# Optimization experiments

Measured on AMD Instinct MI355X. Metric: run time of the kernel, lower is better.

Reference implementation:

```python
import jax, jax.numpy as jnp
import numpy as np

B, T, D, E, TOP_K = 4, 4096, 1024, 8, 2
CAPACITY_FACTOR = 1.5


def setup_inputs() -> dict:
    key = jax.random.key(0)
    k1, k2, k3 = jax.random.split(key, 3)
    x = jax.random.normal(k1, (B, T, D), dtype=jnp.float32)
    Wr = jax.random.normal(k2, (E, D), dtype=jnp.float32) * 0.02   # router weight [E, D]
    We = jax.random.normal(k3, (E, D, D), dtype=jnp.float32) * 0.02  # per-expert dense [E, D, D]
    return {"x": x, "Wr": Wr, "We": We}


def reference(x, Wr, We):
    Bb, Tt, Dd = x.shape
    Ee = Wr.shape[0]
    K = TOP_K
    C = int(Tt * K / Ee * CAPACITY_FACTOR) + 1  # max_tokens_per_expert

    # Router + fused top-k softmax (triton_topk_softmax semantics)
    logits = jnp.einsum('btd,ed->bte', x, Wr)                 # [B, T, E]
    top_vals, top_idx = jax.lax.top_k(logits, K)              # [B, T, K]
    w = jax.nn.softmax(top_vals, axis=-1)                     # [B, T, K]

    # Position of each (token, k) slot inside its expert's capacity buffer,
    # assigned in (t, k) order -- matches the sequential counter in _build_position_map.
    flat_e = top_idx.reshape(Bb, Tt * K)                      # [B, T*K]
    oh = jax.nn.one_hot(flat_e, Ee, dtype=jnp.int32)          # [B, T*K, E]
    pos_all = jnp.cumsum(oh, axis=1) - oh                     # count of earlier slots per expert
    pos = jnp.take_along_axis(pos_all, flat_e[..., None], axis=-1)[..., 0]  # [B, T*K]
    keep = pos < C                                            # capacity drop

    # Scatter tokens into [B, E, C, D] capacity buffers (triton_expert_scatter)
    b_idx = jnp.arange(Bb, dtype=jnp.int32)[:, None]
    dst = (b_idx * Ee + flat_e) * C + pos                     # flat buffer index
    dst = jnp.where(keep, dst, Bb * Ee * C).reshape(-1)       # out-of-range -> dropped
    x_rep = jnp.repeat(x, K, axis=1).reshape(-1, Dd)          # [B*T*K, D]
    buf = jnp.zeros((Bb * Ee * C, Dd), dtype=x.dtype).at[dst].add(x_rep, mode='drop')
    expert_in = buf.reshape(Bb, Ee, C, Dd)

    # expert_fn: per-expert dense layer (grouped GEMM)
    expert_out = jnp.einsum('becd,edf->becf', expert_in, We)  # [B, E, C, D]

    # Gather back + weighted combine (triton_expert_gather)
    gathered = jnp.take(expert_out.reshape(Bb * Ee * C, Dd), dst, axis=0,
                        mode='fill', fill_value=0.0)          # dropped slots -> 0
    gathered = gathered.reshape(Bb, Tt, K, Dd)
    out = jnp.einsum('btk,btkd->btd', w, gathered)            # [B, T, D]
    return out
```

## Files before the change

kernel.cpp:

```cpp
#include <hip/hip_runtime.h>
#include <hip/hip_bf16.h>
#include <math.h>

#define B_ 4
#define T_ 4096
#define D_ 1024
#define E_ 8
#define K_ 2
#define C_ 1537

typedef short bf16x8 __attribute__((ext_vector_type(8)));
typedef float f32x4 __attribute__((ext_vector_type(4)));

__device__ __forceinline__ unsigned short f2bf(float f) {
    union { float f; unsigned int u; } c; c.f = f;
    unsigned int u = c.u;
    return (unsigned short)((u + 0x7fffu + ((u >> 16) & 1u)) >> 16);
}
__device__ __forceinline__ float bf2f(unsigned short u) {
    union { unsigned int i; float f; } c; c.i = ((unsigned int)u) << 16;
    return c.f;
}
__device__ __forceinline__ void ldsdma16(const void* g, void* l) {
    __builtin_amdgcn_global_load_lds((const __attribute__((address_space(1))) void*)g,
                                     (__attribute__((address_space(3))) void*)l, 16, 0, 0);
}

__global__ __launch_bounds__(256) void router_kernel(
    const float* __restrict__ x, const float* __restrict__ Wr,
    unsigned short* __restrict__ xbf, int* __restrict__ top_e,
    float* __restrict__ wbuf) {
    __shared__ float wr_s[E_ * D_];
    int tid = threadIdx.x;
    const float4* wr4 = (const float4*)Wr;
    float4* wrs4 = (float4*)wr_s;
    #pragma unroll
    for (int i = 0; i < 8; i++) wrs4[tid + i * 256] = wr4[tid + i * 256];
    __syncthreads();

    int wave = tid >> 6, lane = tid & 63;
    int h5 = (lane >> 5) & 1, h4 = (lane >> 4) & 1, h3 = (lane >> 3) & 1;

    for (int tt = 0; tt < 4; tt++) {
        int token = blockIdx.x * 16 + wave * 4 + tt;
        const float4* xr = (const float4*)(x + (size_t)token * D_) + lane * 4;
        float xs[16];
        #pragma unroll
        for (int i = 0; i < 4; i++) {
            float4 v = xr[i];
            xs[i * 4 + 0] = v.x; xs[i * 4 + 1] = v.y;
            xs[i * 4 + 2] = v.z; xs[i * 4 + 3] = v.w;
        }
        unsigned short xb[16];
        #pragma unroll
        for (int i = 0; i < 16; i++) xb[i] = f2bf(xs[i]);
        uint4* dst = (uint4*)(xbf + (size_t)token * D_ + lane * 16);
        dst[0] = ((uint4*)xb)[0];
        dst[1] = ((uint4*)xb)[1];

        double acc[E_];
        #pragma unroll
        for (int e = 0; e < E_; e++) {
            const float* wp = wr_s + e * D_ + lane * 16;
            double a = 0.0;
            #pragma unroll
            for (int i = 0; i < 16; i++) a += (double)xs[i] * (double)wp[i];
            acc[e] = a;
        }
        double r4[4];
        #pragma unroll
        for (int i = 0; i < 4; i++) {
            double send = h5 ? acc[i] : acc[4 + i];
            double keep = h5 ? acc[4 + i] : acc[i];
            r4[i] = keep + __shfl_xor(send, 32, 64);
        }
        double r2[2];
        #pragma unroll
        for (int i = 0; i < 2; i++) {
            double send = h4 ? r4[i] : r4[2 + i];
            double keep = h4 ? r4[2 + i] : r4[i];
            r2[i] = keep + __shfl_xor(send, 16, 64);
        }
        double r1;
        {
            double send = h3 ? r2[0] : r2[1];
            double keep = h3 ? r2[1] : r2[0];
            r1 = keep + __shfl_xor(send, 8, 64);
        }
        r1 += __shfl_xor(r1, 4, 64);
        r1 += __shfl_xor(r1, 2, 64);
        r1 += __shfl_xor(r1, 1, 64);
        double le[E_];
        #pragma unroll
        for (int e = 0; e < E_; e++) le[e] = __shfl(r1, e << 3, 64);

        if (lane == 0) {
            int e0 = 0; double v0 = le[0];
            #pragma unroll
            for (int e = 1; e < E_; e++) if (le[e] > v0) { v0 = le[e]; e0 = e; }
            int e1 = -1; double v1 = -1.0e300;
            #pragma unroll
            for (int e = 0; e < E_; e++) if (e != e0 && le[e] > v1) { v1 = le[e]; e1 = e; }
            double ex = exp(v1 - v0);
            top_e[token * 2 + 0] = e0;
            top_e[token * 2 + 1] = e1;
            wbuf[token * 2 + 0] = (float)(1.0 / (1.0 + ex));
            wbuf[token * 2 + 1] = (float)(ex / (1.0 + ex));
        }
    }
}

__global__ __launch_bounds__(256) void wt_kernel(const float* __restrict__ We,
                                                 unsigned short* __restrict__ wtbf) {
    __shared__ unsigned short tile[64][65];
    int e = blockIdx.x >> 8;
    int t = blockIdx.x & 255;
    int d0 = (t >> 4) * 64, f0 = (t & 15) * 64;
    const float* src = We + ((size_t)e * D_ + d0) * D_ + f0;
    int tid = threadIdx.x;
    #pragma unroll
    for (int i = 0; i < 16; i++) {
        int idx = tid + i * 256;
        int r = idx >> 6, c = idx & 63;
        tile[r][c] = f2bf(src[(size_t)r * D_ + c]);
    }
    __syncthreads();
    unsigned short* dstp = wtbf + ((size_t)e * D_ + f0) * D_ + d0;
    #pragma unroll
    for (int i = 0; i < 16; i++) {
        int idx = tid + i * 256;
        int r = idx >> 6, c = idx & 63;
        dstp[(size_t)r * D_ + c] = tile[c][r];
    }
}

__global__ __launch_bounds__(256) void scan_kernel(const int* __restrict__ top_e,
                                                   int* __restrict__ list,
                                                   int* __restrict__ count,
                                                   unsigned char* __restrict__ keep8) {
    int b = blockIdx.x, tid = threadIdx.x;
    const int per = 32;
    __shared__ int cnt[256][9];
    int local[E_];
    #pragma unroll
    for (int e = 0; e < E_; e++) local[e] = 0;
    const int* te = top_e + (size_t)b * 8192 + tid * per;
    int evals[32];
    for (int i = 0; i < per; i++) { evals[i] = te[i]; local[evals[i]]++; }
    #pragma unroll
    for (int e = 0; e < E_; e++) cnt[tid][e] = local[e];
    __syncthreads();

    int wave = tid >> 6, lane = tid & 63;
    #pragma unroll
    for (int ee = 0; ee < 2; ee++) {
        int e = wave * 2 + ee;
        int s0 = cnt[lane * 4 + 0][e], s1 = cnt[lane * 4 + 1][e];
        int s2 = cnt[lane * 4 + 2][e], s3 = cnt[lane * 4 + 3][e];
        int tot = s0 + s1 + s2 + s3;
        int s = tot;
        #pragma unroll
        for (int off = 1; off < 64; off <<= 1) {
            int t2 = __shfl_up(s, off, 64);
            if (lane >= off) s += t2;
        }
        int base = s - tot;
        cnt[lane * 4 + 0][e] = base;
        cnt[lane * 4 + 1][e] = base + s0;
        cnt[lane * 4 + 2][e] = base + s0 + s1;
        cnt[lane * 4 + 3][e] = base + s0 + s1 + s2;
        if (lane == 63) count[b * E_ + e] = min(s, C_);
    }
    __syncthreads();

    int base[E_];
    #pragma unroll
    for (int e = 0; e < E_; e++) base[e] = cnt[tid][e];
    int* lst = list + (size_t)b * E_ * C_;
    unsigned char* kp = keep8 + (size_t)b * 8192;
    for (int i = 0; i < per; i++) {
        int ev = evals[i];
        int p = base[ev]++;
        int slot = tid * per + i;
        kp[slot] = (p < C_) ? 1 : 0;
        if (p < C_) lst[ev * C_ + p] = slot;
    }
}

__global__ __launch_bounds__(256) void gemm_kernel(
    const unsigned short* __restrict__ xbf, const unsigned short* __restrict__ wtbf,
    const int* __restrict__ list, const int* __restrict__ count,
    unsigned short* __restrict__ gbuf) {
    int cb = blockIdx.x;
    int rb = blockIdx.y;
    int pe = blockIdx.z;
    int b = pe >> 3, e = pe & 7;
    int cnt = count[pe];
    int row0 = rb * 128;
    if (row0 >= cnt) return;
    int rows = min(128, cnt - row0);

    __shared__ unsigned short As[128 * 64];
    __shared__ unsigned short Bs[128 * 64];
    __shared__ unsigned int rowByte[128];
    __shared__ int slotArr[128];

    int tid = threadIdx.x;
    if (tid < 128) {
        int slot = list[pe * C_ + row0 + min(tid, rows - 1)];
        slotArr[tid] = (tid < rows) ? slot : -1;
        rowByte[tid] = (unsigned)(((b << 12) + (slot >> 1)) << 11);
    }
    __syncthreads();

    int wave = tid >> 6, lane = tid & 63;
    int quad = lane >> 4, mrow = lane & 15;
    int wm = wave >> 1, wn = wave & 1;

    const char* xbase = (const char*)xbf;
    const char* wtbase = (const char*)wtbf;
    unsigned aAddr[4], bAddr[4];
    #pragma unroll
    for (int i = 0; i < 4; i++) {
        int g = wave * 4 + i;
        int row = (g & 7) * 16 + mrow;
        unsigned kcb = (unsigned)(((g >> 3) * 4 + quad) * 16);
        aAddr[i] = rowByte[row] + kcb;
        int nrow = cb * 128 + row;
        bAddr[i] = (unsigned)((((e << 10) + nrow) << 11) + kcb);
    }

    f32x4 acc[4][4];
    #pragma unroll
    for (int i = 0; i < 4; i++)
        #pragma unroll
        for (int j = 0; j < 4; j++) acc[i][j] = (f32x4){0.f, 0.f, 0.f, 0.f};

    for (int kk = 0; kk < 16; kk++) {
        unsigned ko = (unsigned)kk * 128u;
        __syncthreads();
        #pragma unroll
        for (int i = 0; i < 4; i++) {
            int g = wave * 4 + i;
            ldsdma16(xbase + aAddr[i] + ko, &As[g * 512]);
            ldsdma16(wtbase + bAddr[i] + ko, &Bs[g * 512]);
        }
        __syncthreads();
        #pragma unroll
        for (int ks = 0; ks < 2; ks++) {
            bf16x8 af[4], bfv[4];
            #pragma unroll
            for (int it = 0; it < 4; it++)
                af[it] = *(const bf16x8*)(As + (ks * 8 + wm * 4 + it) * 512 + lane * 8);
            #pragma unroll
            for (int jt = 0; jt < 4; jt++)
                bfv[jt] = *(const bf16x8*)(Bs + (ks * 8 + wn * 4 + jt) * 512 + lane * 8);
            #pragma unroll
            for (int it = 0; it < 4; it++)
                #pragma unroll
                for (int jt = 0; jt < 4; jt++)
                    acc[it][jt] = __builtin_amdgcn_mfma_f32_16x16x32_bf16(
                        af[it], bfv[jt], acc[it][jt], 0, 0, 0);
        }
    }

    int colbase = cb * 128 + wn * 64 + mrow;
    #pragma unroll
    for (int it = 0; it < 4; it++) {
        int mbase = wm * 64 + it * 16 + quad * 4;
        #pragma unroll
        for (int r = 0; r < 4; r++) {
            int slot = slotArr[mbase + r];
            if (slot >= 0) {
                unsigned short* grow = gbuf + ((size_t)((b << 13) + slot) << 10);
                #pragma unroll
                for (int jt = 0; jt < 4; jt++)
                    grow[colbase + jt * 16] = f2bf(acc[it][jt][r]);
            }
        }
    }
}

__global__ __launch_bounds__(256) void combine_kernel(
    const unsigned short* __restrict__ gbuf, const float* __restrict__ wbuf,
    const unsigned char* __restrict__ keep8, float* __restrict__ out) {
    int t = blockIdx.x;
    int b = t >> 12;
    int tid = threadIdx.x;
    int kb = (b << 13) + ((t & 4095) << 1);
    float w0 = wbuf[t * 2 + 0] * (float)keep8[kb + 0];
    float w1 = wbuf[t * 2 + 1] * (float)keep8[kb + 1];
    const ushort4* g0 = (const ushort4*)(gbuf + ((size_t)kb << 10)) + tid;
    const ushort4* g1 = (const ushort4*)(gbuf + (((size_t)kb + 1) << 10)) + tid;
    ushort4 a = *g0, c = *g1;
    float4 o;
    o.x = w0 * bf2f(a.x) + w1 * bf2f(c.x);
    o.y = w0 * bf2f(a.y) + w1 * bf2f(c.y);
    o.z = w0 * bf2f(a.z) + w1 * bf2f(c.z);
    o.w = w0 * bf2f(a.w) + w1 * bf2f(c.w);
    ((float4*)(out + (size_t)t * D_))[tid] = o;
}

extern "C" void kernel_launch(void* const* d_in, const int* in_sizes, int n_in,
                              void* d_out, int out_size, void* d_ws, size_t ws_size,
                              hipStream_t stream) {
    const float* x  = (const float*)d_in[0];
    const float* Wr = (const float*)d_in[1];
    const float* We = (const float*)d_in[2];
    float* out = (float*)d_out;
    char* ws = (char*)d_ws;

    unsigned short* xbf  = (unsigned short*)(ws);
    unsigned short* wtbf = (unsigned short*)(ws + 33554432);
    unsigned short* gbuf = (unsigned short*)(ws + 50331648);
    int*   top_e = (int*)  (ws + 117440512);
    float* wbuf  = (float*)(ws + 117571584);
    int*   list  = (int*)  (ws + 117702656);
    int*   count = (int*)  (ws + 117899392);
    unsigned char* keep8 = (unsigned char*)(ws + 117899520);

    router_kernel<<<dim3(B_ * T_ / 16), dim3(256), 0, stream>>>(x, Wr, xbf, top_e, wbuf);
    wt_kernel<<<dim3(E_ * 256), dim3(256), 0, stream>>>(We, wtbf);
    scan_kernel<<<dim3(B_), dim3(256), 0, stream>>>(top_e, list, count, keep8);
    gemm_kernel<<<dim3(8, 13, 32), dim3(256), 0, stream>>>(xbf, wtbf, list, count, gbuf);
    combine_kernel<<<dim3(B_ * T_), dim3(256), 0, stream>>>(gbuf, wbuf, keep8, out);
}
```

Measured before the change: 353.1 us.

## Fuse router and weight-transpose kernels; use persistent work-queue GEMM and grid-stride combine

The router and weight-transpose kernels are merged into one launch by partitioning block IDs. The scan kernel's last block builds a prefix table of non-empty tiles per (batch, expert). The GEMM becomes a persistent kernel that pulls tile indices from an atomic counter, so no blocks are launched for empty capacity rows. The combine kernel switches to a fixed grid with a grid-stride loop. These changes cut launch overhead and idle blocks, at the cost of atomic contention and extra per-tile setup in the GEMM.

```diff
diff --git a/kernel.cpp b/kernel.cpp
--- a/kernel.cpp
+++ b/kernel.cpp
@@ -26,118 +26,121 @@
                                      (__attribute__((address_space(3))) void*)l, 16, 0, 0);
 }
 
-__global__ __launch_bounds__(256) void router_kernel(
+__global__ __launch_bounds__(256) void prep_kernel(
     const float* __restrict__ x, const float* __restrict__ Wr,
-    unsigned short* __restrict__ xbf, int* __restrict__ top_e,
-    float* __restrict__ wbuf) {
-    __shared__ float wr_s[E_ * D_];
+    const float* __restrict__ We,
+    unsigned short* __restrict__ xbf, unsigned short* __restrict__ wtbf,
+    int* __restrict__ top_e, float* __restrict__ wbuf, int* __restrict__ qctl) {
+    __shared__ char smem[32768];
     int tid = threadIdx.x;
-    const float4* wr4 = (const float4*)Wr;
-    float4* wrs4 = (float4*)wr_s;
-    #pragma unroll
-    for (int i = 0; i < 8; i++) wrs4[tid + i * 256] = wr4[tid + i * 256];
-    __syncthreads();
-
-    int wave = tid >> 6, lane = tid & 63;
-    int h5 = (lane >> 5) & 1, h4 = (lane >> 4) & 1, h3 = (lane >> 3) & 1;
-
-    for (int tt = 0; tt < 4; tt++) {
-        int token = blockIdx.x * 16 + wave * 4 + tt;
-        const float4* xr = (const float4*)(x + (size_t)token * D_) + lane * 4;
-        float xs[16];
-        #pragma unroll
-        for (int i = 0; i < 4; i++) {
-            float4 v = xr[i];
-            xs[i * 4 + 0] = v.x; xs[i * 4 + 1] = v.y;
-            xs[i * 4 + 2] = v.z; xs[i * 4 + 3] = v.w;
-        }
-        unsigned short xb[16];
-        #pragma unroll
-        for (int i = 0; i < 16; i++) xb[i] = f2bf(xs[i]);
-        uint4* dst = (uint4*)(xbf + (size_t)token * D_ + lane * 16);
-        dst[0] = ((uint4*)xb)[0];
-        dst[1] = ((uint4*)xb)[1];
-
-        double acc[E_];
-        #pragma unroll
-        for (int e = 0; e < E_; e++) {
-            const float* wp = wr_s + e * D_ + lane * 16;
-            double a = 0.0;
-            #pragma unroll
-            for (int i = 0; i < 16; i++) a += (double)xs[i] * (double)wp[i];
-            acc[e] = a;
-        }
-        double r4[4];
-        #pragma unroll
-        for (int i = 0; i < 4; i++) {
-            double send = h5 ? acc[i] : acc[4 + i];
-            double keep = h5 ? acc[4 + i] : acc[i];
-            r4[i] = keep + __shfl_xor(send, 32, 64);
-        }
-        double r2[2];
-        #pragma unroll
-        for (int i = 0; i < 2; i++) {
-            double send = h4 ? r4[i] : r4[2 + i];
-            double keep = h4 ? r4[2 + i] : r4[i];
-            r2[i] = keep + __shfl_xor(send, 16, 64);
-        }
-        double r1;
-        {
-            double send = h3 ? r2[0] : r2[1];
-            double keep = h3 ? r2[1] : r2[0];
-            r1 = keep + __shfl_xor(send, 8, 64);
-        }
-        r1 += __shfl_xor(r1, 4, 64);
-        r1 += __shfl_xor(r1, 2, 64);
-        r1 += __shfl_xor(r1, 1, 64);
-        double le[E_];
-        #pragma unroll
-        for (int e = 0; e < E_; e++) le[e] = __shfl(r1, e << 3, 64);
-
-        if (lane == 0) {
-            int e0 = 0; double v0 = le[0];
-            #pragma unroll
-            for (int e = 1; e < E_; e++) if (le[e] > v0) { v0 = le[e]; e0 = e; }
-            int e1 = -1; double v1 = -1.0e300;
-            #pragma unroll
-            for (int e = 0; e < E_; e++) if (e != e0 && le[e] > v1) { v1 = le[e]; e1 = e; }
-            double ex = exp(v1 - v0);
-            top_e[token * 2 + 0] = e0;
-            top_e[token * 2 + 1] = e1;
-            wbuf[token * 2 + 0] = (float)(1.0 / (1.0 + ex));
-            wbuf[token * 2 + 1] = (float)(ex / (1.0 + ex));
-        }
-    }
-}
-
-__global__ __launch_bounds__(256) void wt_kernel(const float* __restrict__ We,
-                                                 unsigned short* __restrict__ wtbf) {
-    __shared__ unsigned short tile[64][65];
-    int e = blockIdx.x >> 8;
-    int t = blockIdx.x & 255;
-    int d0 = (t >> 4) * 64, f0 = (t & 15) * 64;
-    const float* src = We + ((size_t)e * D_ + d0) * D_ + f0;
-    int tid = threadIdx.x;
-    #pragma unroll
-    for (int i = 0; i < 16; i++) {
-        int idx = tid + i * 256;
-        int r = idx >> 6, c = idx & 63;
-        tile[r][c] = f2bf(src[(size_t)r * D_ + c]);
-    }
-    __syncthreads();
-    unsigned short* dstp = wtbf + ((size_t)e * D_ + f0) * D_ + d0;
-    #pragma unroll
-    for (int i = 0; i < 16; i++) {
-        int idx = tid + i * 256;
-        int r = idx >> 6, c = idx & 63;
-        dstp[(size_t)r * D_ + c] = tile[c][r];
+    if (blockIdx.x < 1024) {
+        if (blockIdx.x == 0 && tid == 0) { qctl[0] = 0; qctl[1] = 0; }
+        float* wr_s = (float*)smem;
+        const float4* wr4 = (const float4*)Wr;
+        float4* wrs4 = (float4*)wr_s;
+        #pragma unroll
+        for (int i = 0; i < 8; i++) wrs4[tid + i * 256] = wr4[tid + i * 256];
+        __syncthreads();
+
+        int wave = tid >> 6, lane = tid & 63;
+        int h5 = (lane >> 5) & 1, h4 = (lane >> 4) & 1, h3 = (lane >> 3) & 1;
+
+        for (int tt = 0; tt < 4; tt++) {
+            int token = blockIdx.x * 16 + wave * 4 + tt;
+            const float4* xr = (const float4*)(x + (size_t)token * D_) + lane * 4;
+            float xs[16];
+            #pragma unroll
+            for (int i = 0; i < 4; i++) {
+                float4 v = xr[i];
+                xs[i * 4 + 0] = v.x; xs[i * 4 + 1] = v.y;
+                xs[i * 4 + 2] = v.z; xs[i * 4 + 3] = v.w;
+            }
+            unsigned short xb[16];
+            #pragma unroll
+            for (int i = 0; i < 16; i++) xb[i] = f2bf(xs[i]);
+            uint4* dst = (uint4*)(xbf + (size_t)token * D_ + lane * 16);
+            dst[0] = ((uint4*)xb)[0];
+            dst[1] = ((uint4*)xb)[1];
+
+            double acc[E_];
+            #pragma unroll
+            for (int e = 0; e < E_; e++) {
+                const float* wp = wr_s + e * D_ + lane * 16;
+                double a = 0.0;
+                #pragma unroll
+                for (int i = 0; i < 16; i++) a += (double)xs[i] * (double)wp[i];
+                acc[e] = a;
+            }
+            double r4[4];
+            #pragma unroll
+            for (int i = 0; i < 4; i++) {
+                double send = h5 ? acc[i] : acc[4 + i];
+                double keep = h5 ? acc[4 + i] : acc[i];
+                r4[i] = keep + __shfl_xor(send, 32, 64);
+            }
+            double r2[2];
+            #pragma unroll
+            for (int i = 0; i < 2; i++) {
+                double send = h4 ? r4[i] : r4[2 + i];
+                double keep = h4 ? r4[2 + i] : r4[i];
+                r2[i] = keep + __shfl_xor(send, 16, 64);
+            }
+            double r1;
+            {
+                double send = h3 ? r2[0] : r2[1];
+                double keep = h3 ? r2[1] : r2[0];
+                r1 = keep + __shfl_xor(send, 8, 64);
+            }
+            r1 += __shfl_xor(r1, 4, 64);
+            r1 += __shfl_xor(r1, 2, 64);
+            r1 += __shfl_xor(r1, 1, 64);
+            double le[E_];
+            #pragma unroll
+            for (int e = 0; e < E_; e++) le[e] = __shfl(r1, e << 3, 64);
+
+            if (lane == 0) {
+                int e0 = 0; double v0 = le[0];
+                #pragma unroll
+                for (int e = 1; e < E_; e++) if (le[e] > v0) { v0 = le[e]; e0 = e; }
+                int e1 = -1; double v1 = -1.0e300;
+                #pragma unroll
+                for (int e = 0; e < E_; e++) if (e != e0 && le[e] > v1) { v1 = le[e]; e1 = e; }
+                double ex = exp(v1 - v0);
+                top_e[token * 2 + 0] = e0;
+                top_e[token * 2 + 1] = e1;
+                wbuf[token * 2 + 0] = (float)(1.0 / (1.0 + ex));
+                wbuf[token * 2 + 1] = (float)(ex / (1.0 + ex));
+            }
+        }
+    } else {
+        unsigned short (*tile)[65] = (unsigned short(*)[65])smem;
+        int bid = blockIdx.x - 1024;
+        int e = bid >> 8;
+        int t = bid & 255;
+        int d0 = (t >> 4) * 64, f0 = (t & 15) * 64;
+        const float* src = We + ((size_t)e * D_ + d0) * D_ + f0;
+        #pragma unroll
+        for (int i = 0; i < 16; i++) {
+            int idx = tid + i * 256;
+            int r = idx >> 6, c = idx & 63;
+            tile[r][c] = f2bf(src[(size_t)r * D_ + c]);
+        }
+        __syncthreads();
+        unsigned short* dstp = wtbf + ((size_t)e * D_ + f0) * D_ + d0;
+        #pragma unroll
+        for (int i = 0; i < 16; i++) {
+            int idx = tid + i * 256;
+            int r = idx >> 6, c = idx & 63;
+            dstp[(size_t)r * D_ + c] = tile[c][r];
+        }
     }
 }
 
 __global__ __launch_bounds__(256) void scan_kernel(const int* __restrict__ top_e,
                                                    int* __restrict__ list,
                                                    int* __restrict__ count,
-                                                   unsigned char* __restrict__ keep8) {
+                                                   unsigned char* __restrict__ keep8,
+                                                   int* __restrict__ qctl) {
     int b = blockIdx.x, tid = threadIdx.x;
     const int per = 32;
     __shared__ int cnt[256][9];
@@ -185,97 +188,129 @@
         kp[slot] = (p < C_) ? 1 : 0;
         if (p < C_) lst[ev * C_ + p] = slot;
     }
-}
-
-__global__ __launch_bounds__(256) void gemm_kernel(
+    __syncthreads();
+    if (tid == 0) {
+        __threadfence();
+        if (atomicAdd(&qctl[1], 1) == B_ - 1) {
+            __threadfence();
+            int run = 0;
+            qctl[8] = 0;
+            for (int pe = 0; pe < B_ * E_; pe++) {
+                int c = count[pe];
+                run += ((c + 127) >> 7) * 8;
+                qctl[9 + pe] = run;
+            }
+            qctl[2] = run;
+            __threadfence();
+        }
+    }
+}
+
+__global__ __launch_bounds__(256, 4) void gemm_kernel(
     const unsigned short* __restrict__ xbf, const unsigned short* __restrict__ wtbf,
     const int* __restrict__ list, const int* __restrict__ count,
-    unsigned short* __restrict__ gbuf) {
-    int cb = blockIdx.x;
-    int rb = blockIdx.y;
-    int pe = blockIdx.z;
-    int b = pe >> 3, e = pe & 7;
-    int cnt = count[pe];
-    int row0 = rb * 128;
-    if (row0 >= cnt) return;
-    int rows = min(128, cnt - row0);
-
+    int* __restrict__ qctl, unsigned short* __restrict__ gbuf) {
     __shared__ unsigned short As[128 * 64];
     __shared__ unsigned short Bs[128 * 64];
     __shared__ unsigned int rowByte[128];
     __shared__ int slotArr[128];
+    __shared__ int prefS[33];
+    __shared__ int countS[32];
+    __shared__ int itemS;
 
     int tid = threadIdx.x;
-    if (tid < 128) {
-        int slot = list[pe * C_ + row0 + min(tid, rows - 1)];
-        slotArr[tid] = (tid < rows) ? slot : -1;
-        rowByte[tid] = (unsigned)(((b << 12) + (slot >> 1)) << 11);
-    }
-    __syncthreads();
+    if (tid < 33) prefS[tid] = qctl[8 + tid];
+    if (tid >= 64 && tid < 96) countS[tid - 64] = count[tid - 64];
+    int total = qctl[2];
 
     int wave = tid >> 6, lane = tid & 63;
     int quad = lane >> 4, mrow = lane & 15;
     int wm = wave >> 1, wn = wave & 1;
-
     const char* xbase = (const char*)xbf;
     const char* wtbase = (const char*)wtbf;
-    unsigned aAddr[4], bAddr[4];
-    #pragma unroll
-    for (int i = 0; i < 4; i++) {
-        int g = wave * 4 + i;
-        int row = (g & 7) * 16 + mrow;
-        unsigned kcb = (unsigned)(((g >> 3) * 4 + quad) * 16);
-        aAddr[i] = rowByte[row] + kcb;
-        int nrow = cb * 128 + row;
-        bAddr[i] = (unsigned)((((e << 10) + nrow) << 11) + kcb);
-    }
-
-    f32x4 acc[4][4];
-    #pragma unroll
-    for (int i = 0; i < 4; i++)
-        #pragma unroll
-        for (int j = 0; j < 4; j++) acc[i][j] = (f32x4){0.f, 0.f, 0.f, 0.f};
-
-    for (int kk = 0; kk < 16; kk++) {
-        unsigned ko = (unsigned)kk * 128u;
+
+    while (true) {
+        if (tid == 0) itemS = atomicAdd(&qctl[0], 1);
         __syncthreads();
+        int item = itemS;
+        if (item >= total) break;
+
+        int pe = 0;
+        #pragma unroll
+        for (int p = 1; p < 32; p++) pe += (item >= prefS[p]) ? 1 : 0;
+        int local = item - prefS[pe];
+        int rb = local >> 3;
+        int cb = local & 7;
+        int b = pe >> 3, e = pe & 7;
+        int cnt = countS[pe];
+        int row0 = rb * 128;
+        int rows = min(128, cnt - row0);
+
+        if (tid < 128) {
+            int slot = list[pe * C_ + row0 + min(tid, rows - 1)];
+            slotArr[tid] = (tid < rows) ? slot : -1;
+            rowByte[tid] = (unsigned)(((b << 12) + (slot >> 1)) << 11);
+        }
+        __syncthreads();
+
+        unsigned aAddr[4], bAddr[4];
         #pragma unroll
         for (int i = 0; i < 4; i++) {
             int g = wave * 4 + i;
-            ldsdma16(xbase + aAddr[i] + ko, &As[g * 512]);
-            ldsdma16(wtbase + bAddr[i] + ko, &Bs[g * 512]);
-        }
-        __syncthreads();
-        #pragma unroll
-        for (int ks = 0; ks < 2; ks++) {
-            bf16x8 af[4], bfv[4];
-            #pragma unroll
-            for (int it = 0; it < 4; it++)
-                af[it] = *(const bf16x8*)(As + (ks * 8 + wm * 4 + it) * 512 + lane * 8);
-            #pragma unroll
-            for (int jt = 0; jt < 4; jt++)
-                bfv[jt] = *(const bf16x8*)(Bs + (ks * 8 + wn * 4 + jt) * 512 + lane * 8);
-            #pragma unroll
-            for (int it = 0; it < 4; it++)
+            int row = (g & 7) * 16 + mrow;
+            unsigned kcb = (unsigned)(((g >> 3) * 4 + quad) * 16);
+            aAddr[i] = rowByte[row] + kcb;
+            int nrow = cb * 128 + row;
+            bAddr[i] = (unsigned)((((e << 10) + nrow) << 11) + kcb);
+        }
+
+        f32x4 acc[4][4];
+        #pragma unroll
+        for (int i = 0; i < 4; i++)
+            #pragma unroll
+            for (int j = 0; j < 4; j++) acc[i][j] = (f32x4){0.f, 0.f, 0.f, 0.f};
+
+        for (int kk = 0; kk < 16; kk++) {
+            unsigned ko = (unsigned)kk * 128u;
+            __syncthreads();
+            #pragma unroll
+            for (int i = 0; i < 4; i++) {
+                int g = wave * 4 + i;
+                ldsdma16(xbase + aAddr[i] + ko, &As[g * 512]);
+                ldsdma16(wtbase + bAddr[i] + ko, &Bs[g * 512]);
+            }
+            __syncthreads();
+            #pragma unroll
+            for (int ks = 0; ks < 2; ks++) {
+                bf16x8 af[4], bfv[4];
+                #pragma unroll
+                for (int it = 0; it < 4; it++)
+                    af[it] = *(const bf16x8*)(As + (ks * 8 + wm * 4 + it) * 512 + lane * 8);
                 #pragma unroll
                 for (int jt = 0; jt < 4; jt++)
-                    acc[it][jt] = __builtin_amdgcn_mfma_f32_16x16x32_bf16(
-                        af[it], bfv[jt], acc[it][jt], 0, 0, 0);
-        }
-    }
-
-    int colbase = cb * 128 + wn * 64 + mrow;
-    #pragma unroll
-    for (int it = 0; it < 4; it++) {
-        int mbase = wm * 64 + it * 16 + quad * 4;
-        #pragma unroll
-        for (int r = 0; r < 4; r++) {
-            int slot = slotArr[mbase + r];
-            if (slot >= 0) {
-                unsigned short* grow = gbuf + ((size_t)((b << 13) + slot) << 10);
-                #pragma unroll
-                for (int jt = 0; jt < 4; jt++)
-                    grow[colbase + jt * 16] = f2bf(acc[it][jt][r]);
+                    bfv[jt] = *(const bf16x8*)(Bs + (ks * 8 + wn * 4 + jt) * 512 + lane * 8);
+                #pragma unroll
+                for (int it = 0; it < 4; it++)
+                    #pragma unroll
+                    for (int jt = 0; jt < 4; jt++)
+                        acc[it][jt] = __builtin_amdgcn_mfma_f32_16x16x32_bf16(
+                            af[it], bfv[jt], acc[it][jt], 0, 0, 0);
+            }
+        }
+
+        int colbase = cb * 128 + wn * 64 + mrow;
+        #pragma unroll
+        for (int it = 0; it < 4; it++) {
+            int mbase = wm * 64 + it * 16 + quad * 4;
+            #pragma unroll
+            for (int r = 0; r < 4; r++) {
+                int slot = slotArr[mbase + r];
+                if (slot >= 0) {
+                    unsigned short* grow = gbuf + ((size_t)((b << 13) + slot) << 10);
+                    #pragma unroll
+                    for (int jt = 0; jt < 4; jt++)
+                        grow[colbase + jt * 16] = f2bf(acc[it][jt][r]);
+                }
             }
         }
     }
@@ -284,21 +319,24 @@
 __global__ __launch_bounds__(256) void combine_kernel(
     const unsigned short* __restrict__ gbuf, const float* __restrict__ wbuf,
     const unsigned char* __restrict__ keep8, float* __restrict__ out) {
-    int t = blockIdx.x;
-    int b = t >> 12;
-    int tid = threadIdx.x;
-    int kb = (b << 13) + ((t & 4095) << 1);
-    float w0 = wbuf[t * 2 + 0] * (float)keep8[kb + 0];
-    float w1 = wbuf[t * 2 + 1] * (float)keep8[kb + 1];
-    const ushort4* g0 = (const ushort4*)(gbuf + ((size_t)kb << 10)) + tid;
-    const ushort4* g1 = (const ushort4*)(gbuf + (((size_t)kb + 1) << 10)) + tid;
-    ushort4 a = *g0, c = *g1;
-    float4 o;
-    o.x = w0 * bf2f(a.x) + w1 * bf2f(c.x);
-    o.y = w0 * bf2f(a.y) + w1 * bf2f(c.y);
-    o.z = w0 * bf2f(a.z) + w1 * bf2f(c.z);
-    o.w = w0 * bf2f(a.w) + w1 * bf2f(c.w);
-    ((float4*)(out + (size_t)t * D_))[tid] = o;
+    const int NV = B_ * T_ * (D_ / 4);
+    int stride = gridDim.x * blockDim.x;
+    for (int i = blockIdx.x * blockDim.x + threadIdx.x; i < NV; i += stride) {
+        int t = i >> 8;
+        int ch = i & 255;
+        int b = t >> 12;
+        int kb = (b << 13) + ((t & 4095) << 1);
+        float w0 = wbuf[t * 2 + 0] * (float)keep8[kb + 0];
+        float w1 = wbuf[t * 2 + 1] * (float)keep8[kb + 1];
+        ushort4 a = ((const ushort4*)(gbuf + ((size_t)kb << 10)))[ch];
+        ushort4 c = ((const ushort4*)(gbuf + (((size_t)kb + 1) << 10)))[ch];
+        float4 o;
+        o.x = w0 * bf2f(a.x) + w1 * bf2f(c.x);
+        o.y = w0 * bf2f(a.y) + w1 * bf2f(c.y);
+        o.z = w0 * bf2f(a.z) + w1 * bf2f(c.z);
+        o.w = w0 * bf2f(a.w) + w1 * bf2f(c.w);
+        ((float4*)(out + (size_t)t * D_))[ch] = o;
+    }
 }
 
 extern "C" void kernel_launch(void* const* d_in, const int* in_sizes, int n_in,
@@ -317,11 +355,12 @@
     float* wbuf  = (float*)(ws + 117571584);
     int*   list  = (int*)  (ws + 117702656);
     int*   count = (int*)  (ws + 117899392);
-    unsigned char* keep8 = (unsigned char*)(ws + 117899520);
-
-    router_kernel<<<dim3(B_ * T_ / 16), dim3(256), 0, stream>>>(x, Wr, xbf, top_e, wbuf);
-    wt_kernel<<<dim3(E_ * 256), dim3(256), 0, stream>>>(We, wtbf);
-    scan_kernel<<<dim3(B_), dim3(256), 0, stream>>>(top_e, list, count, keep8);
-    gemm_kernel<<<dim3(8, 13, 32), dim3(256), 0, stream>>>(xbf, wtbf, list, count, gbuf);
-    combine_kernel<<<dim3(B_ * T_), dim3(256), 0, stream>>>(gbuf, wbuf, keep8, out);
-}
+    unsigned char* keep8 = (unsigned char*)(ws + 117899648);
+    int*   qctl  = (int*)  (ws + 117932416);
+
+    prep_kernel<<<dim3(1024 + 2048), dim3(256), 0, stream>>>(x, Wr, We, xbf, wtbf,
+                                                             top_e, wbuf, qctl);
+    scan_kernel<<<dim3(B_), dim3(256), 0, stream>>>(top_e, list, count, keep8, qctl);
+    gemm_kernel<<<dim3(1024), dim3(256), 0, stream>>>(xbf, wtbf, list, count, qctl, gbuf);
+    combine_kernel<<<dim3(1024), dim3(256), 0, stream>>>(gbuf, wbuf, keep8, out);
+}
```

Result: slower. 360.7 us (+2.2%).
